# Performance work log

Measured on AMD Instinct MI355X. Metric: run time of the kernel, lower is better.

Reference implementation:

```python
import jax, jax.numpy as jnp
import numpy as np
from jax import lax

D_MODEL = 1024
FFN = 4096
CHUNK = 256
TTT_LR = 0.01
KSIZE = 5


def setup_inputs() -> dict:
    key = jax.random.key(0)
    ks = jax.random.split(key, 7)
    B, T = 2, 4096
    x = jax.random.normal(ks[0], (B, T, D_MODEL), dtype=jnp.float32)
    ttt_target = jax.random.normal(ks[1], (B, T, D_MODEL), dtype=jnp.float32)
    w_gate_up = jax.random.normal(ks[2], (2 * FFN, D_MODEL), dtype=jnp.float32) * 0.02
    w_down = jax.random.normal(ks[3], (D_MODEL, FFN), dtype=jnp.float32) * 0.02
    ttt_proj = jax.random.normal(ks[4], (D_MODEL, D_MODEL), dtype=jnp.float32) * 0.02
    conv_w = jax.random.normal(ks[5], (D_MODEL, 1, KSIZE), dtype=jnp.float32) * 0.02
    conv_b = jax.random.normal(ks[6], (D_MODEL,), dtype=jnp.float32) * 0.02
    return {"x": x, "ttt_target": ttt_target, "w_gate_up": w_gate_up,
            "w_down": w_down, "ttt_proj": ttt_proj, "conv_w": conv_w, "conv_b": conv_b}


def _pad_and_chunk(a, chunk):
    B, T, D = a.shape
    pad = (-T) % chunk
    if pad:
        a = jnp.pad(a, ((0, 0), (0, pad), (0, 0)))
    return a.reshape(B, -1, chunk, D)


def reference(x, ttt_target, w_gate_up, w_down, ttt_proj, conv_w, conv_b):
    B, T, D = x.shape
    # SwiGLU up path
    gate_up = jnp.einsum('btd,fd->btf', x, w_gate_up)  # (B,T,2F)
    gate, up = jnp.split(gate_up, 2, axis=-1)
    h = jax.nn.silu(gate) * up  # (B,T,F)
    # causal depthwise conv on ttt_target (torch pads K-1 both sides then slices [:T])
    t_ncl = ttt_target.transpose(0, 2, 1)  # (B,D,T)
    t = lax.conv_general_dilated(
        t_ncl, conv_w, window_strides=(1,), padding=[(KSIZE - 1, 0)],
        dimension_numbers=('NCH', 'OIH', 'NCH'), feature_group_count=D)
    t = (t + conv_b[None, :, None]).transpose(0, 2, 1)  # (B,T,D)
    # chunk
    h_c = _pad_and_chunk(h, CHUNK)  # (B,nc,C,F)
    t_c = _pad_and_chunk(t, CHUNK)  # (B,nc,C,D)
    nc = h_c.shape[1]
    if nc > 1:
        t_proj = jnp.einsum('btcd,ed->btce', t_c[:, :-1], ttt_proj)  # (B,nc-1,C,D)
        d_down = jnp.einsum('btch,btcd->btdh', h_c[:, :-1], t_proj)  # (B,nc-1,D,F)
    else:
        d_down = jnp.zeros((B, 0, D, FFN), dtype=h.dtype)
    w_orig = jnp.broadcast_to(w_down[None, None], (B, 1, D, FFN))
    w_all = jnp.concatenate([w_orig, d_down * jnp.float32(TTT_LR)], axis=1)
    w_adapted = jnp.cumsum(w_all, axis=1)  # (B,nc,D,F)
    out = jnp.einsum('btdh,btch->btcd', w_adapted, h_c)  # (B,nc,C,D)
    return out.reshape(B, -1, D)[:, :T]
```

## Files before the change

kernel.cpp:

```cpp
#include <hip/hip_runtime.h>
#include <hip/hip_bf16.h>
#include <stdint.h>

typedef unsigned short ushort_t;
typedef __bf16 bf16x8 __attribute__((ext_vector_type(8)));
typedef float f32x16 __attribute__((ext_vector_type(16)));

#define BM 128
#define BN 128
#define BK 64

__device__ inline float b2f(ushort_t u) {
    unsigned int x = ((unsigned int)u) << 16;
    float f; __builtin_memcpy(&f, &x, 4); return f;
}
__device__ inline ushort_t f2b(float f) {
    unsigned int x; __builtin_memcpy(&x, &f, 4);
    unsigned int r = (x + 0x7FFFu + ((x >> 16) & 1u)) >> 16;
    return (ushort_t)r;
}
__device__ inline void stage16(const ushort_t* g, ushort_t* s) {
    __builtin_amdgcn_global_load_lds((const __attribute__((address_space(1))) void*)g,
                                     (__attribute__((address_space(3))) void*)s, 16, 0, 0);
}
__device__ inline int swz(int r) { return (r & 7) ^ ((r >> 3) & 3); }
__device__ inline void stage_tile(const ushort_t* G, int ld, int k0, ushort_t* S, int tid) {
#pragma unroll
    for (int t = 0; t < 4; ++t) {
        int e = tid + t * 256;
        int row = e >> 3;
        int sw = ((e & 7) ^ swz(row)) * 8;
        stage16(G + (long long)row * ld + k0 + sw, &S[e * 8]);
    }
}
__device__ inline bf16x8 ldfrag(const ushort_t* S, int r, int c) {
    return *(const bf16x8*)&S[r * BK + ((c ^ swz(r)) * 8)];
}
__device__ inline void tile_decode(int& m0, int& n0) {
    const int nx = gridDim.x;
    int lin = blockIdx.y * nx + blockIdx.x;
    if ((nx & 7) == 0) {
        int q = nx >> 3;
        int k = lin & 7, s = lin >> 3;
        n0 = (k * q + s % q) * BN;
        m0 = (s / q) * BM;
    } else {
        m0 = blockIdx.y * BM;
        n0 = blockIdx.x * BN;
    }
}


#define SBAR() __builtin_amdgcn_sched_barrier(0)
#define BARRIER() do { SBAR(); __builtin_amdgcn_s_barrier(); SBAR(); } while (0)
#define WAITV(N) asm volatile("s_waitcnt vmcnt(" #N ")" ::: "memory")

__device__ inline int sw2(int r) { return ((r) & 3) ^ ((r >> 3) & 3); }

__device__ inline void stage_half(const ushort_t* G, int ldg, int kElem,
                                  ushort_t* Sbuf, int h, int tid) {
#pragma unroll
    for (int i2 = 0; i2 < 2; ++i2) {
        int s = tid + i2 * 512;
        int r = s >> 2, q = s & 3;
        int c = 4 * h + (q ^ sw2(r));
        stage16(G + (long long)r * ldg + kElem + c * 8, Sbuf + h * 8192 + s * 8);
    }
}
__device__ inline void stage_halfA(const ushort_t* G, int ldg,
                                   ushort_t* Sbuf, int h, int tid) {
    int r = tid >> 2, q = tid & 3;
    int c = 4 * h + (q ^ sw2(r));
    stage16(G + (long long)r * ldg + c * 8, Sbuf + h * 4096 + tid * 8);
}
__device__ inline int frag_off(int r, int c) {
    return r * 32 + ((c ^ sw2(r)) & 3) * 8;
}

template <int KS0, int MI0, bool LB>
__device__ __forceinline__ void phase_load(const ushort_t* cA, const ushort_t* cB,
                                           const int oa[4][2], const int ob[2][2],
                                           bf16x8 af_[2][2], bf16x8 bf_[2][2]) {
    constexpr int HO = (KS0 >> 1) * 8192;
#pragma unroll
    for (int k2 = 0; k2 < 2; ++k2) {
#pragma unroll
        for (int m2 = 0; m2 < 2; ++m2)
            af_[m2][k2] = *(const bf16x8*)&cA[oa[MI0 + m2][k2] + HO];
        if (LB) {
#pragma unroll
            for (int n2 = 0; n2 < 2; ++n2)
                bf_[n2][k2] = *(const bf16x8*)&cB[ob[n2][k2] + HO];
        }
    }
}
template <int MI0>
__device__ __forceinline__ void phase_mfma(bf16x8 af_[2][2], bf16x8 bf_[2][2],
                                           f32x16 (&acc)[4][2]) {
#pragma unroll
    for (int k2 = 0; k2 < 2; ++k2)
#pragma unroll
        for (int m2 = 0; m2 < 2; ++m2)
#pragma unroll
            for (int n2 = 0; n2 < 2; ++n2)
                acc[MI0 + m2][n2] = __builtin_amdgcn_mfma_f32_32x32x16_bf16(
                    af_[m2][k2], bf_[n2][k2], acc[MI0 + m2][n2], 0, 0, 0);
}

__device__ __forceinline__ void gemm256_core(const ushort_t* __restrict__ Ag, int lda,
                                             const ushort_t* __restrict__ Bg, int ldb,
                                             int K, ushort_t* smem, int tid,
                                             int wr, int wc, int l32, int hl,
                                             f32x16 (&acc)[4][2]) {
    ushort_t* A0s = smem;
    ushort_t* A1s = smem + 16384;
    ushort_t* B0s = smem + 32768;
    ushort_t* B1s = smem + 49152;
    const int NT = K >> 6;

    int oa[4][2], ob[2][2];
#pragma unroll
    for (int m2 = 0; m2 < 4; ++m2)
#pragma unroll
        for (int k2 = 0; k2 < 2; ++k2)
            oa[m2][k2] = frag_off(wr * 128 + m2 * 32 + l32, k2 * 2 + hl);
#pragma unroll
    for (int n2 = 0; n2 < 2; ++n2)
#pragma unroll
        for (int k2 = 0; k2 < 2; ++k2)
            ob[n2][k2] = frag_off(wc * 64 + n2 * 32 + l32, k2 * 2 + hl);

    stage_half(Ag, lda, 0, A0s, 0, tid);
    stage_half(Bg, ldb, 0, B0s, 0, tid);
    stage_half(Ag, lda, 0, A0s, 1, tid);
    stage_half(Bg, ldb, 0, B0s, 1, tid);
    stage_half(Ag, lda, 64, A1s, 0, tid);
    stage_half(Bg, ldb, 64, B1s, 0, tid);
    WAITV(8);
    BARRIER();

    for (int kt = 0; kt < NT; ++kt) {
        ushort_t* cA = (kt & 1) ? A1s : A0s;
        ushort_t* cB = (kt & 1) ? B1s : B0s;
        ushort_t* nA = (kt & 1) ? A0s : A1s;
        ushort_t* nB = (kt & 1) ? B0s : B1s;
        const bool h1 = (kt + 1 < NT), h2 = (kt + 2 < NT);
        const int kE1 = (kt + 1) << 6, kE2 = (kt + 2) << 6;
        bf16x8 af_[2][2], bf_[2][2];
        if (h1) stage_half(Ag, lda, kE1, nA, 1, tid);
        phase_load<0, 0, true>(cA, cB, oa, ob, af_, bf_);
        __builtin_amdgcn_s_setprio(1);
        phase_mfma<0>(af_, bf_, acc);
        __builtin_amdgcn_s_setprio(0);
        BARRIER();
        if (h1) stage_half(Bg, ldb, kE1, nB, 1, tid);
        phase_load<0, 2, false>(cA, cB, oa, ob, af_, bf_);
        __builtin_amdgcn_s_setprio(1);
        phase_mfma<2>(af_, bf_, acc);
        __builtin_amdgcn_s_setprio(0);
        if (h1) { WAITV(8); } else { WAITV(0); }
        BARRIER();
        if (h2) stage_half(Ag, lda, kE2, cA, 0, tid);
        phase_load<2, 0, true>(cA, cB, oa, ob, af_, bf_);
        __builtin_amdgcn_s_setprio(1);
        phase_mfma<0>(af_, bf_, acc);
        __builtin_amdgcn_s_setprio(0);
        BARRIER();
        if (h2) stage_half(Bg, ldb, kE2, cB, 0, tid);
        phase_load<2, 2, false>(cA, cB, oa, ob, af_, bf_);
        __builtin_amdgcn_s_setprio(1);
        phase_mfma<2>(af_, bf_, acc);
        __builtin_amdgcn_s_setprio(0);
        if (h1) { if (h2) { WAITV(8); } else { WAITV(4); } }
        BARRIER();
    }
}

__global__ __launch_bounds__(512, 2)
void k_gemm256_silu(const ushort_t* __restrict__ A, const ushort_t* __restrict__ Bp,
                    ushort_t* __restrict__ H) {
    extern __shared__ __attribute__((aligned(16))) ushort_t smem2[];
    const int tid = threadIdx.x;
    const int lane = tid & 63, l32 = lane & 31, hl = lane >> 5;
    const int wv = tid >> 6, wr = wv >> 2, wc = wv & 3;
    int lin = blockIdx.y * 32 + blockIdx.x;
    int k8 = lin & 7, s = lin >> 3;
    int n0 = (k8 * 4 + (s & 3)) * 256;
    int m0 = (s >> 2) * 256;
    const ushort_t* Ag = A + (long long)m0 * 1024;
    const ushort_t* Bg = Bp + (long long)n0 * 1024;
    f32x16 acc[4][2];
#pragma unroll
    for (int i = 0; i < 4; ++i) { acc[i][0] = (f32x16)(0.f); acc[i][1] = (f32x16)(0.f); }
    gemm256_core(Ag, 1024, Bg, 1024, 1024, smem2, tid, wr, wc, l32, hl, acc);
    const int hc = (n0 >> 1) + wc * 32 + l32;
#pragma unroll
    for (int mi = 0; mi < 4; ++mi)
#pragma unroll
        for (int reg = 0; reg < 16; ++reg) {
            int row = m0 + wr * 128 + mi * 32 + (reg & 3) + 8 * (reg >> 2) + 4 * hl;
            float g = acc[mi][0][reg], u = acc[mi][1][reg];
            float sg = g / (1.f + __expf(-g));
            H[(long long)row * 4096 + hc] = f2b(sg * u);
        }
}

__global__ __launch_bounds__(512, 2)
void k_gemm256_tri(const ushort_t* __restrict__ Hh, ushort_t* __restrict__ P) {
    extern __shared__ __attribute__((aligned(16))) ushort_t smem2[];
    const int tid = threadIdx.x;
    const int lane = tid & 63, l32 = lane & 31, hl = lane >> 5;
    const int wv = tid >> 6, wr = wv >> 2, wc = wv & 3;
    int pairIdx = (blockIdx.x & 7) * 30 + (blockIdx.x >> 3);
    const int bb = pairIdx / 120;
    int p = pairIdx % 120;
    int i = 1, rem = p;
    while (rem >= i) { rem -= i; ++i; }
    const int j = rem;
    const ushort_t* Ag = Hh + (long long)bb * 4096 * 4096 + (long long)(i * 256) * 4096;
    const ushort_t* Bg = Hh + (long long)bb * 4096 * 4096 + (long long)(j * 256) * 4096;
    f32x16 acc[4][2];
#pragma unroll
    for (int a = 0; a < 4; ++a) { acc[a][0] = (f32x16)(0.f); acc[a][1] = (f32x16)(0.f); }
    gemm256_core(Ag, 4096, Bg, 4096, 4096, smem2, tid, wr, wc, l32, hl, acc);
    ushort_t* Pp = P + (long long)bb * 4096 * 4096;
#pragma unroll
    for (int mi = 0; mi < 4; ++mi)
#pragma unroll
        for (int nj = 0; nj < 2; ++nj) {
            int col = j * 256 + wc * 64 + nj * 32 + l32;
#pragma unroll
            for (int reg = 0; reg < 16; ++reg) {
                int row = i * 256 + wr * 128 + mi * 32 + (reg & 3) + 8 * (reg >> 2) + 4 * hl;
                Pp[(long long)row * 4096 + col] = f2b(acc[mi][nj][reg]);
            }
        }
}

template <int KS0>
__device__ __forceinline__ void oload_ks(const ushort_t* cA, const ushort_t* cB,
                                         const int oa[2][2], const int ob[2][2],
                                         bf16x8 af_[2][2], bf16x8 bf_[2][2]) {
    constexpr int HOA = (KS0 >> 1) * 4096;
    constexpr int HOB = (KS0 >> 1) * 8192;
#pragma unroll
    for (int k2 = 0; k2 < 2; ++k2) {
#pragma unroll
        for (int m2 = 0; m2 < 2; ++m2)
            af_[m2][k2] = *(const bf16x8*)&cA[oa[m2][k2] + HOA];
#pragma unroll
        for (int n2 = 0; n2 < 2; ++n2)
            bf_[n2][k2] = *(const bf16x8*)&cB[ob[n2][k2] + HOB];
    }
}
__device__ __forceinline__ void omfma(bf16x8 af_[2][2], bf16x8 bf_[2][2],
                                      f32x16 (&acc)[2][2]) {
#pragma unroll
    for (int k2 = 0; k2 < 2; ++k2)
#pragma unroll
        for (int m2 = 0; m2 < 2; ++m2)
#pragma unroll
            for (int n2 = 0; n2 < 2; ++n2)
                acc[m2][n2] = __builtin_amdgcn_mfma_f32_32x32x16_bf16(
                    af_[m2][k2], bf_[n2][k2], acc[m2][n2], 0, 0, 0);
}

__global__ __launch_bounds__(512, 2)
void k_gemm256_out(const ushort_t* __restrict__ h, const ushort_t* __restrict__ wdown,
                   const ushort_t* __restrict__ P, const ushort_t* __restrict__ tpT,
                   float* __restrict__ out) {
    constexpr int T = 4096, D = 1024, F = 4096, C = 256, K1 = 4096;
    extern __shared__ __attribute__((aligned(16))) ushort_t smem2[];
    const int tid = threadIdx.x;
    const int lane = tid & 63, l32 = lane & 31, hl = lane >> 5;
    const int wv = tid >> 6, wr = wv >> 2, wc = wv & 3;

    const int bx = blockIdx.x;
    const int logical = (bx & 7) * 32 + (bx >> 3);
    const int z = logical >> 3, t = logical & 7;
    const int bb = z >> 4, ii = z & 15;
    const int m0 = (t >> 2) * 128, n0 = (t & 3) * 256;
    const int K = K1 + ii * C;

    const ushort_t* hA = h + (long long)bb * T * F + (long long)(ii * C + m0) * F;
    const ushort_t* pA = P + (long long)bb * T * T + (long long)(ii * C + m0) * T;
    const ushort_t* wB = wdown + (long long)n0 * F;
    const ushort_t* tB = tpT + (long long)bb * D * T + (long long)n0 * T;

    ushort_t* A0s = smem2;
    ushort_t* A1s = smem2 + 8192;
    ushort_t* B0s = smem2 + 16384;
    ushort_t* B1s = smem2 + 32768;

    int oa[2][2], ob[2][2];
#pragma unroll
    for (int m2 = 0; m2 < 2; ++m2)
#pragma unroll
        for (int k2 = 0; k2 < 2; ++k2)
            oa[m2][k2] = frag_off(wr * 64 + m2 * 32 + l32, k2 * 2 + hl);
#pragma unroll
    for (int n2 = 0; n2 < 2; ++n2)
#pragma unroll
        for (int k2 = 0; k2 < 2; ++k2)
            ob[n2][k2] = frag_off(wc * 64 + n2 * 32 + l32, k2 * 2 + hl);

    f32x16 acc[2][2];
#pragma unroll
    for (int a = 0; a < 2; ++a)
#pragma unroll
        for (int c = 0; c < 2; ++c) acc[a][c] = (f32x16)(0.f);

    auto srcA = [&](int kE) { return kE < K1 ? hA + kE : pA + (kE - K1); };
    auto srcB = [&](int kE) { return kE < K1 ? wB + kE : tB + (kE - K1); };

    const int NT = K >> 6;

    stage_halfA(srcA(0), F, A0s, 0, tid);
    stage_half (srcB(0), F, 0, B0s, 0, tid);
    stage_halfA(srcA(0), F, A0s, 1, tid);
    stage_half (srcB(0), F, 0, B0s, 1, tid);
    stage_halfA(srcA(64), F, A1s, 0, tid);
    stage_half (srcB(64), F, 0, B1s, 0, tid);
    WAITV(6);
    BARRIER();

    for (int kt = 0; kt < NT; ++kt) {
        ushort_t* cA = (kt & 1) ? A1s : A0s;
        ushort_t* cB = (kt & 1) ? B1s : B0s;
        ushort_t* nA = (kt & 1) ? A0s : A1s;
        ushort_t* nB = (kt & 1) ? B0s : B1s;
        const bool h1 = (kt + 1 < NT), h2 = (kt + 2 < NT);
        const int kE1 = (kt + 1) << 6, kE2 = (kt + 2) << 6;
        bf16x8 af_[2][2], bf_[2][2];
        if (h1) {
            stage_halfA(srcA(kE1), F, nA, 1, tid);
            stage_half (srcB(kE1), F, 0, nB, 1, tid);
        }
        oload_ks<0>(cA, cB, oa, ob, af_, bf_);
        __builtin_amdgcn_s_setprio(1);
        omfma(af_, bf_, acc);
        __builtin_amdgcn_s_setprio(0);
        if (h1) { WAITV(6); } else { WAITV(0); }
        BARRIER();
        if (h2) {
            stage_halfA(srcA(kE2), F, cA, 0, tid);
            stage_half (srcB(kE2), F, 0, cB, 0, tid);
        }
        oload_ks<2>(cA, cB, oa, ob, af_, bf_);
        __builtin_amdgcn_s_setprio(1);
        omfma(af_, bf_, acc);
        __builtin_amdgcn_s_setprio(0);
        if (h2) { WAITV(6); } else { if (h1) { WAITV(3); } else { WAITV(0); } }
        BARRIER();
    }

    float* Op = out + (long long)bb * T * D + (long long)(ii * C) * D;
#pragma unroll
    for (int mi = 0; mi < 2; ++mi)
#pragma unroll
        for (int nj = 0; nj < 2; ++nj) {
            int col = n0 + wc * 64 + nj * 32 + l32;
#pragma unroll
            for (int reg = 0; reg < 16; ++reg) {
                int row = m0 + wr * 64 + mi * 32 + (reg & 3) + 8 * (reg >> 2) + 4 * hl;
                Op[(long long)row * D + col] = acc[mi][nj][reg];
            }
        }
}

__global__ void k_prep(const float* __restrict__ x, const float* __restrict__ wgu,
                       const float* __restrict__ proj, const float* __restrict__ wdown,
                       const float* __restrict__ tt, const float* __restrict__ cw,
                       const float* __restrict__ cb,
                       ushort_t* __restrict__ xb, ushort_t* __restrict__ gb,
                       ushort_t* __restrict__ pb, ushort_t* __restrict__ wb,
                       ushort_t* __restrict__ tb, int permW) {
    constexpr int T = 4096, D = 1024;
    int blk = blockIdx.x;
    if (blk < 21504) {
        int i = blk * 256 + threadIdx.x;
        const float* src; ushort_t* dst; int off; int dstoff;
        if (i < 2097152)      { src = x;     dst = xb; off = i; dstoff = off; }
        else if (i < 4194304) {
            src = wgu; dst = gb; off = i - 2097152;
            if (permW) {
                int r = off >> 8, cu = off & 255;
                int pr = (r < 4096) ? (((r >> 5) << 6) + (r & 31))
                                    : ((((r - 4096) >> 5) << 6) + 32 + ((r - 4096) & 31));
                dstoff = (pr << 8) + cu;
            } else dstoff = off;
        }
        else if (i < 4456448) { src = proj;  dst = pb; off = i - 4194304; dstoff = off; }
        else                  { src = wdown; dst = wb; off = i - 4456448; dstoff = off; }
        float4 v = ((const float4*)src)[off];
        ushort4 o; o.x = f2b(v.x); o.y = f2b(v.y); o.z = f2b(v.z); o.w = f2b(v.w);
        ((ushort4*)dst)[dstoff] = o;
    } else {
        int idx = (blk - 21504) * 256 + threadIdx.x;
        int d = idx & (D - 1);
        int tq = (idx >> 10) & (T / 4 - 1);
        int b = idx / (D * (T / 4));
        int t0 = tq * 4;
        const float* base = tt + (long long)b * T * D + d;
        float w0 = cw[d * 5 + 0], w1 = cw[d * 5 + 1], w2 = cw[d * 5 + 2],
              w3 = cw[d * 5 + 3], w4 = cw[d * 5 + 4];
        float bias = cb[d];
        float win[8];
#pragma unroll
        for (int m = 0; m < 8; ++m) {
            int ts = t0 - 4 + m;
            win[m] = (ts >= 0) ? base[(long long)ts * D] : 0.f;
        }
        ushort_t* op = tb + (long long)b * T * D + (long long)t0 * D + d;
#pragma unroll
        for (int r = 0; r < 4; ++r) {
            float a = bias + w0 * win[r] + w1 * win[r + 1] + w2 * win[r + 2]
                    + w3 * win[r + 3] + w4 * win[r + 4];
            op[(long long)r * D] = f2b(a);
        }
    }
}

__global__ __launch_bounds__(256, 4)
void k_gemm_nt(const ushort_t* __restrict__ A, const ushort_t* __restrict__ B,
               ushort_t* __restrict__ C, int K, int lda, int ldb, int ldc,
               long long sAb, long long sBb, long long sCb, float scale) {
    __shared__ __attribute__((aligned(16))) ushort_t sA[BM * BK];
    __shared__ __attribute__((aligned(16))) ushort_t sB[BN * BK];

    int m0, n0;
    tile_decode(m0, n0);
    const int bb = blockIdx.z;
    const ushort_t* Ab = A + bb * sAb + (long long)m0 * lda;
    const ushort_t* Bb = B + bb * sBb + (long long)n0 * ldb;

    const int tid = threadIdx.x;
    const int lane = tid & 63, l32 = lane & 31, half = lane >> 5;
    const int wave = tid >> 6;
    const int wm = (wave >> 1) * 64, wn = (wave & 1) * 64;

    f32x16 acc[2][2];
#pragma unroll
    for (int i = 0; i < 2; ++i)
#pragma unroll
        for (int j = 0; j < 2; ++j) acc[i][j] = (f32x16)(0.f);

    for (int k0 = 0; k0 < K; k0 += BK) {
        __syncthreads();
        stage_tile(Ab, lda, k0, sA, tid);
        stage_tile(Bb, ldb, k0, sB, tid);
        __syncthreads();
#pragma unroll
        for (int ks = 0; ks < 4; ++ks) {
            bf16x8 af[2], bfr[2];
#pragma unroll
            for (int mi = 0; mi < 2; ++mi)
                af[mi] = ldfrag(sA, wm + mi * 32 + l32, ks * 2 + half);
#pragma unroll
            for (int nj = 0; nj < 2; ++nj)
                bfr[nj] = ldfrag(sB, wn + nj * 32 + l32, ks * 2 + half);
#pragma unroll
            for (int mi = 0; mi < 2; ++mi)
#pragma unroll
                for (int nj = 0; nj < 2; ++nj)
                    acc[mi][nj] = __builtin_amdgcn_mfma_f32_32x32x16_bf16(af[mi], bfr[nj], acc[mi][nj], 0, 0, 0);
        }
    }

    ushort_t* Cp = C + bb * sCb;
#pragma unroll
    for (int mi = 0; mi < 2; ++mi)
#pragma unroll
        for (int nj = 0; nj < 2; ++nj) {
            int col = n0 + wn + nj * 32 + l32;
#pragma unroll
            for (int reg = 0; reg < 16; ++reg) {
                int row = m0 + wm + mi * 32 + (reg & 3) + 8 * (reg >> 2) + 4 * half;
                Cp[(long long)row * ldc + col] = f2b(acc[mi][nj][reg] * scale);
            }
        }
}

__global__ __launch_bounds__(256)
void k_gemm_silu(const ushort_t* __restrict__ A, const ushort_t* __restrict__ Bg,
                 const ushort_t* __restrict__ Bu, ushort_t* __restrict__ H,
                 int K, int lda, int ldb, int ldh) {
    __shared__ __attribute__((aligned(16))) ushort_t sA[BM * BK];
    __shared__ __attribute__((aligned(16))) ushort_t sBg[BN * BK];
    __shared__ __attribute__((aligned(16))) ushort_t sBu[BN * BK];

    int m0, n0;
    tile_decode(m0, n0);
    const ushort_t* Ab = A + (long long)m0 * lda;
    const ushort_t* Bgb = Bg + (long long)n0 * ldb;
    const ushort_t* Bub = Bu + (long long)n0 * ldb;

    const int tid = threadIdx.x;
    const int lane = tid & 63, l32 = lane & 31, half = lane >> 5;
    const int wave = tid >> 6;
    const int wm = (wave >> 1) * 64, wn = (wave & 1) * 64;

    f32x16 ag[2][2], au[2][2];
#pragma unroll
    for (int i = 0; i < 2; ++i)
#pragma unroll
        for (int j = 0; j < 2; ++j) { ag[i][j] = (f32x16)(0.f); au[i][j] = (f32x16)(0.f); }

    for (int k0 = 0; k0 < K; k0 += BK) {
        __syncthreads();
        stage_tile(Ab, lda, k0, sA, tid);
        stage_tile(Bgb, ldb, k0, sBg, tid);
        stage_tile(Bub, ldb, k0, sBu, tid);
        __syncthreads();
#pragma unroll
        for (int ks = 0; ks < 4; ++ks) {
            bf16x8 af[2], bg[2], bu[2];
#pragma unroll
            for (int mi = 0; mi < 2; ++mi)
                af[mi] = ldfrag(sA, wm + mi * 32 + l32, ks * 2 + half);
#pragma unroll
            for (int nj = 0; nj < 2; ++nj) {
                bg[nj] = ldfrag(sBg, wn + nj * 32 + l32, ks * 2 + half);
                bu[nj] = ldfrag(sBu, wn + nj * 32 + l32, ks * 2 + half);
            }
#pragma unroll
            for (int mi = 0; mi < 2; ++mi)
#pragma unroll
                for (int nj = 0; nj < 2; ++nj) {
                    ag[mi][nj] = __builtin_amdgcn_mfma_f32_32x32x16_bf16(af[mi], bg[nj], ag[mi][nj], 0, 0, 0);
                    au[mi][nj] = __builtin_amdgcn_mfma_f32_32x32x16_bf16(af[mi], bu[nj], au[mi][nj], 0, 0, 0);
                }
        }
    }

#pragma unroll
    for (int mi = 0; mi < 2; ++mi)
#pragma unroll
        for (int nj = 0; nj < 2; ++nj) {
            int col = n0 + wn + nj * 32 + l32;
#pragma unroll
            for (int reg = 0; reg < 16; ++reg) {
                int row = m0 + wm + mi * 32 + (reg & 3) + 8 * (reg >> 2) + 4 * half;
                float g = ag[mi][nj][reg], u = au[mi][nj][reg];
                float s = g / (1.f + __expf(-g));
                H[(long long)row * ldh + col] = f2b(s * u);
            }
        }
}

__global__ __launch_bounds__(256, 4)
void k_gemm_tri(const ushort_t* __restrict__ H, ushort_t* __restrict__ P,
                int K, int ldh, int ldp, long long sHb, long long sPb) {
    __shared__ __attribute__((aligned(16))) ushort_t sA[BM * BK];
    __shared__ __attribute__((aligned(16))) ushort_t sB[BN * BK];

    const int lin = blockIdx.x;
    const int g = lin >> 5, w = lin & 31;
    const int xk = w & 7, t = w >> 3;
    int pairIdx = g * 8 + xk;
    const int bb = pairIdx / 120;
    int p = pairIdx % 120;
    int i = 1, rem = p;
    while (rem >= i) { rem -= i; ++i; }
    const int j = rem;
    const int m0 = (t >> 1) * BM, n0 = (t & 1) * BN;

    const ushort_t* Ab = H + bb * sHb + (long long)(i * 256 + m0) * ldh;
    const ushort_t* Bb = H + bb * sHb + (long long)(j * 256 + n0) * ldh;

    const int tid = threadIdx.x;
    const int lane = tid & 63, l32 = lane & 31, half = lane >> 5;
    const int wave = tid >> 6;
    const int wm = (wave >> 1) * 64, wn = (wave & 1) * 64;

    f32x16 acc[2][2];
#pragma unroll
    for (int a = 0; a < 2; ++a)
#pragma unroll
        for (int c = 0; c < 2; ++c) acc[a][c] = (f32x16)(0.f);

    for (int k0 = 0; k0 < K; k0 += BK) {
        __syncthreads();
        stage_tile(Ab, ldh, k0, sA, tid);
        stage_tile(Bb, ldh, k0, sB, tid);
        __syncthreads();
#pragma unroll
        for (int ks = 0; ks < 4; ++ks) {
            bf16x8 af[2], bfr[2];
#pragma unroll
            for (int mi = 0; mi < 2; ++mi)
                af[mi] = ldfrag(sA, wm + mi * 32 + l32, ks * 2 + half);
#pragma unroll
            for (int nj = 0; nj < 2; ++nj)
                bfr[nj] = ldfrag(sB, wn + nj * 32 + l32, ks * 2 + half);
#pragma unroll
            for (int mi = 0; mi < 2; ++mi)
#pragma unroll
                for (int nj = 0; nj < 2; ++nj)
                    acc[mi][nj] = __builtin_amdgcn_mfma_f32_32x32x16_bf16(af[mi], bfr[nj], acc[mi][nj], 0, 0, 0);
        }
    }

    ushort_t* Pp = P + bb * sPb;
#pragma unroll
    for (int mi = 0; mi < 2; ++mi)
#pragma unroll
        for (int nj = 0; nj < 2; ++nj) {
            int col = j * 256 + n0 + wn + nj * 32 + l32;
#pragma unroll
            for (int reg = 0; reg < 16; ++reg) {
                int row = i * 256 + m0 + wm + mi * 32 + (reg & 3) + 8 * (reg >> 2) + 4 * half;
                Pp[(long long)row * ldp + col] = f2b(acc[mi][nj][reg]);
            }
        }
}

__global__ __launch_bounds__(256, 4)
void k_gemm_out(const ushort_t* __restrict__ h, const ushort_t* __restrict__ wdown,
                const ushort_t* __restrict__ P, const ushort_t* __restrict__ tpT,
                float* __restrict__ out) {
    constexpr int T = 4096, D = 1024, F = 4096, C = 256, K1 = 4096;
    __shared__ __attribute__((aligned(16))) ushort_t sA[BM * BK];
    __shared__ __attribute__((aligned(16))) ushort_t sB[BN * BK];

    const int z = blockIdx.z, bb = z >> 4, ii = z & 15;
    const int K2 = ii * C;
    int m0, n0;
    tile_decode(m0, n0);

    const ushort_t* A1 = h + (long long)bb * T * F + (long long)(ii * C + m0) * F;
    const ushort_t* B1 = wdown + (long long)n0 * F;
    const ushort_t* A2 = P + (long long)bb * T * T + (long long)(ii * C + m0) * T;
    const ushort_t* B2 = tpT + (long long)bb * D * T + (long long)n0 * T;

    const int tid = threadIdx.x;
    const int lane = tid & 63, l32 = lane & 31, half = lane >> 5;
    const int wave = tid >> 6;
    const int wm = (wave >> 1) * 64, wn = (wave & 1) * 64;

    f32x16 acc[2][2];
#pragma unroll
    for (int i = 0; i < 2; ++i)
#pragma unroll
        for (int j = 0; j < 2; ++j) acc[i][j] = (f32x16)(0.f);

    const int K = K1 + K2;
    for (int k0 = 0; k0 < K; k0 += BK) {
        const ushort_t* As = (k0 < K1) ? A1 + k0 : A2 + (k0 - K1);
        const ushort_t* Bs = (k0 < K1) ? B1 + k0 : B2 + (k0 - K1);
        __syncthreads();
        stage_tile(As, 4096, 0, sA, tid);
        stage_tile(Bs, 4096, 0, sB, tid);
        __syncthreads();
#pragma unroll
        for (int ks = 0; ks < 4; ++ks) {
            bf16x8 af[2], bfr[2];
#pragma unroll
            for (int mi = 0; mi < 2; ++mi)
                af[mi] = ldfrag(sA, wm + mi * 32 + l32, ks * 2 + half);
#pragma unroll
            for (int nj = 0; nj < 2; ++nj)
                bfr[nj] = ldfrag(sB, wn + nj * 32 + l32, ks * 2 + half);
#pragma unroll
            for (int mi = 0; mi < 2; ++mi)
#pragma unroll
                for (int nj = 0; nj < 2; ++nj)
                    acc[mi][nj] = __builtin_amdgcn_mfma_f32_32x32x16_bf16(af[mi], bfr[nj], acc[mi][nj], 0, 0, 0);
        }
    }

    float* Op = out + (long long)bb * T * D + (long long)ii * C * D;
#pragma unroll
    for (int mi = 0; mi < 2; ++mi)
#pragma unroll
        for (int nj = 0; nj < 2; ++nj) {
            int col = n0 + wn + nj * 32 + l32;
#pragma unroll
            for (int reg = 0; reg < 16; ++reg) {
                int row = m0 + wm + mi * 32 + (reg & 3) + 8 * (reg >> 2) + 4 * half;
                Op[(long long)row * D + col] = acc[mi][nj][reg];
            }
        }
}

static int g_big = -1;

extern "C" void kernel_launch(void* const* d_in, const int* in_sizes, int n_in,
                              void* d_out, int out_size, void* d_ws, size_t ws_size,
                              hipStream_t stream) {
    const float* x         = (const float*)d_in[0];
    const float* ttt_tgt   = (const float*)d_in[1];
    const float* w_gate_up = (const float*)d_in[2];
    const float* w_down    = (const float*)d_in[3];
    const float* ttt_proj  = (const float*)d_in[4];
    const float* conv_w    = (const float*)d_in[5];
    const float* conv_b    = (const float*)d_in[6];
    float* out = (float*)d_out;
    (void)in_sizes; (void)n_in; (void)out_size; (void)ws_size;

    constexpr int Bb = 2, T = 4096, D = 1024, F = 4096, C = 256;
    constexpr float LR = 0.01f;

    if (g_big < 0) {
        hipError_t e1 = hipFuncSetAttribute((const void*)k_gemm256_silu,
                                            hipFuncAttributeMaxDynamicSharedMemorySize, 131072);
        hipError_t e2 = hipFuncSetAttribute((const void*)k_gemm256_tri,
                                            hipFuncAttributeMaxDynamicSharedMemorySize, 131072);
        hipError_t e3 = hipFuncSetAttribute((const void*)k_gemm256_out,
                                            hipFuncAttributeMaxDynamicSharedMemorySize, 98304);
        g_big = (e1 == hipSuccess && e2 == hipSuccess && e3 == hipSuccess) ? 1 : 0;
    }

    char* ws = (char*)d_ws;
    ushort_t* x_bf     = (ushort_t*)(ws);
    ushort_t* wgu_bf   = (ushort_t*)(ws + 16777216LL);
    ushort_t* t_bf     = (ushort_t*)(ws + 2 * 16777216LL);
    ushort_t* P        = (ushort_t*)(ws);
    ushort_t* proj_bf  = (ushort_t*)(ws + 67108864LL);
    ushort_t* wdown_bf = (ushort_t*)(ws + 67108864LL + 2097152LL);
    ushort_t* tpT      = (ushort_t*)(ws + 67108864LL + 2097152LL + 8388608LL);
    ushort_t* h        = (ushort_t*)(ws + 67108864LL + 2097152LL + 8388608LL + 16777216LL);

    k_prep<<<21504 + 8192, 256, 0, stream>>>(x, w_gate_up, ttt_proj, w_down,
                                             ttt_tgt, conv_w, conv_b,
                                             x_bf, wgu_bf, proj_bf, wdown_bf, t_bf, g_big);

    k_gemm_nt<<<dim3(T / BN, D / BM, Bb), 256, 0, stream>>>(
        proj_bf, t_bf, tpT, D, D, D, T,
        0, (long long)T * D, (long long)D * T, LR);

    if (g_big) {
        k_gemm256_silu<<<dim3(32, 32, 1), 512, 131072, stream>>>(x_bf, wgu_bf, h);
    } else {
        k_gemm_silu<<<dim3(F / BN, (Bb * T) / BM, 1), 256, 0, stream>>>(
            x_bf, wgu_bf, wgu_bf + (long long)F * D, h, D, D, D, F);
    }

    if (g_big) {
        k_gemm256_tri<<<dim3(240, 1, 1), 512, 131072, stream>>>(h, P);
    } else {
        k_gemm_tri<<<dim3(960, 1, 1), 256, 0, stream>>>(
            h, P, F, F, T, (long long)T * F, (long long)T * T);
    }

    if (g_big) {
        k_gemm256_out<<<dim3(256, 1, 1), 512, 98304, stream>>>(h, wdown_bf, P, tpT, out);
    } else {
        k_gemm_out<<<dim3(D / BN, C / BM, Bb * 16), 256, 0, stream>>>(
            h, wdown_bf, P, tpT, out);
    }
}
```

Measured before the change: 570.3 us.

## Split the output GEMM's K dimension in two with atomic accumulation

The output GEMM now launches twice as many blocks, each covering half of the K range (the w_down part plus the triangular P part), and accumulates partial tiles into the output with float atomicAdd. The output is zeroed with a memset beforehand. This is meant to fill more of the device and reduce tail imbalance from the varying K lengths per chunk, at the cost of an extra memset pass and atomic write traffic to the output.

Result: slower. 603.4 us (+5.8%).

```diff
diff --git a/kernel.cpp b/kernel.cpp
--- a/kernel.cpp
+++ b/kernel.cpp
@@ -276,11 +276,17 @@
     const int wv = tid >> 6, wr = wv >> 2, wc = wv & 3;
 
     const int bx = blockIdx.x;
-    const int logical = (bx & 7) * 32 + (bx >> 3);
-    const int z = logical >> 3, t = logical & 7;
+    const int logical = (bx & 7) * 64 + (bx >> 3);
+    const int z = logical >> 4;
+    const int t = (logical >> 1) & 7;
+    const int seg = logical & 1;
     const int bb = z >> 4, ii = z & 15;
     const int m0 = (t >> 2) * 128, n0 = (t & 3) * 256;
     const int K = K1 + ii * C;
+    const int NT = K >> 6;
+    const int NTh = NT >> 1;
+    const int ktBeg = seg ? NTh : 0;
+    const int NTs = seg ? (NT - NTh) : NTh;
 
     const ushort_t* hA = h + (long long)bb * T * F + (long long)(ii * C + m0) * F;
     const ushort_t* pA = P + (long long)bb * T * T + (long long)(ii * C + m0) * T;
@@ -313,24 +319,24 @@
     auto srcA = [&](int kE) { return kE < K1 ? hA + kE : pA + (kE - K1); };
     auto srcB = [&](int kE) { return kE < K1 ? wB + kE : tB + (kE - K1); };
 
-    const int NT = K >> 6;
-
-    stage_halfA(srcA(0), F, A0s, 0, tid);
-    stage_half (srcB(0), F, 0, B0s, 0, tid);
-    stage_halfA(srcA(0), F, A0s, 1, tid);
-    stage_half (srcB(0), F, 0, B0s, 1, tid);
-    stage_halfA(srcA(64), F, A1s, 0, tid);
-    stage_half (srcB(64), F, 0, B1s, 0, tid);
+    const int kE0 = ktBeg << 6;
+
+    stage_halfA(srcA(kE0), F, A0s, 0, tid);
+    stage_half (srcB(kE0), F, 0, B0s, 0, tid);
+    stage_halfA(srcA(kE0), F, A0s, 1, tid);
+    stage_half (srcB(kE0), F, 0, B0s, 1, tid);
+    stage_halfA(srcA(kE0 + 64), F, A1s, 0, tid);
+    stage_half (srcB(kE0 + 64), F, 0, B1s, 0, tid);
     WAITV(6);
     BARRIER();
 
-    for (int kt = 0; kt < NT; ++kt) {
+    for (int kt = 0; kt < NTs; ++kt) {
         ushort_t* cA = (kt & 1) ? A1s : A0s;
         ushort_t* cB = (kt & 1) ? B1s : B0s;
         ushort_t* nA = (kt & 1) ? A0s : A1s;
         ushort_t* nB = (kt & 1) ? B0s : B1s;
-        const bool h1 = (kt + 1 < NT), h2 = (kt + 2 < NT);
-        const int kE1 = (kt + 1) << 6, kE2 = (kt + 2) << 6;
+        const bool h1 = (kt + 1 < NTs), h2 = (kt + 2 < NTs);
+        const int kE1 = (ktBeg + kt + 1) << 6, kE2 = (ktBeg + kt + 2) << 6;
         bf16x8 af_[2][2], bf_[2][2];
         if (h1) {
             stage_halfA(srcA(kE1), F, nA, 1, tid);
@@ -363,7 +369,7 @@
 #pragma unroll
             for (int reg = 0; reg < 16; ++reg) {
                 int row = m0 + wr * 64 + mi * 32 + (reg & 3) + 8 * (reg >> 2) + 4 * hl;
-                Op[(long long)row * D + col] = acc[mi][nj][reg];
+                atomicAdd(&Op[(long long)row * D + col], acc[mi][nj][reg]);
             }
         }
 }
@@ -696,7 +702,7 @@
     const float* conv_w    = (const float*)d_in[5];
     const float* conv_b    = (const float*)d_in[6];
     float* out = (float*)d_out;
-    (void)in_sizes; (void)n_in; (void)out_size; (void)ws_size;
+    (void)in_sizes; (void)n_in; (void)ws_size;
 
     constexpr int Bb = 2, T = 4096, D = 1024, F = 4096, C = 256;
     constexpr float LR = 0.01f;
@@ -721,6 +727,8 @@
     ushort_t* tpT      = (ushort_t*)(ws + 67108864LL + 2097152LL + 8388608LL);
     ushort_t* h        = (ushort_t*)(ws + 67108864LL + 2097152LL + 8388608LL + 16777216LL);
 
+    if (g_big) hipMemsetAsync(out, 0, (size_t)out_size, stream);
+
     k_prep<<<21504 + 8192, 256, 0, stream>>>(x, w_gate_up, ttt_proj, w_down,
                                              ttt_tgt, conv_w, conv_b,
                                              x_bf, wgu_bf, proj_bf, wdown_bf, t_bf, g_big);
@@ -744,7 +752,7 @@
     }
 
     if (g_big) {
-        k_gemm256_out<<<dim3(256, 1, 1), 512, 98304, stream>>>(h, wdown_bf, P, tpT, out);
+        k_gemm256_out<<<dim3(512, 1, 1), 512, 98304, stream>>>(h, wdown_bf, P, tpT, out);
     } else {
         k_gemm_out<<<dim3(D / BN, C / BM, Bb * 16), 256, 0, stream>>>(
             h, wdown_bf, P, tpT, out);
```

## Replace double-buffered 64-wide K pipeline with 4-slot ring of 32-wide stages

Applied to the files above, without the earlier changes.

Both GEMM cores (the SwiGLU/P GEMM and the output GEMM) drop the two-buffer, 64-element K tile with split half-phase loads. They now use a four-slot circular buffer of 32-element K slices, prefetched three slices ahead. Each iteration issues one slice load, then does all fragment reads and MFMAs for the current slice, then waits and hits one barrier. The aim is to keep more global loads in flight and simplify synchronization. The cost is more barriers per unit of K and smaller MFMA batches between barriers, with the same shared memory footprint.

Measured after the change: 563.7 us. No clear change (-1.2%).

```diff
diff --git a/kernel.cpp b/kernel.cpp
--- a/kernel.cpp
+++ b/kernel.cpp
@@ -58,53 +58,22 @@
 __device__ inline int sw2(int r) { return ((r) & 3) ^ ((r >> 3) & 3); }
 
 __device__ inline void stage_half(const ushort_t* G, int ldg, int kElem,
-                                  ushort_t* Sbuf, int h, int tid) {
+                                  ushort_t* Sbuf, int tid) {
 #pragma unroll
     for (int i2 = 0; i2 < 2; ++i2) {
         int s = tid + i2 * 512;
         int r = s >> 2, q = s & 3;
-        int c = 4 * h + (q ^ sw2(r));
-        stage16(G + (long long)r * ldg + kElem + c * 8, Sbuf + h * 8192 + s * 8);
-    }
-}
-__device__ inline void stage_halfA(const ushort_t* G, int ldg,
-                                   ushort_t* Sbuf, int h, int tid) {
+        int c = q ^ sw2(r);
+        stage16(G + (long long)r * ldg + kElem + c * 8, Sbuf + s * 8);
+    }
+}
+__device__ inline void stage_halfA(const ushort_t* G, int ldg, ushort_t* Sbuf, int tid) {
     int r = tid >> 2, q = tid & 3;
-    int c = 4 * h + (q ^ sw2(r));
-    stage16(G + (long long)r * ldg + c * 8, Sbuf + h * 4096 + tid * 8);
+    int c = q ^ sw2(r);
+    stage16(G + (long long)r * ldg + c * 8, Sbuf + tid * 8);
 }
 __device__ inline int frag_off(int r, int c) {
     return r * 32 + ((c ^ sw2(r)) & 3) * 8;
-}
-
-template <int KS0, int MI0, bool LB>
-__device__ __forceinline__ void phase_load(const ushort_t* cA, const ushort_t* cB,
-                                           const int oa[4][2], const int ob[2][2],
-                                           bf16x8 af_[2][2], bf16x8 bf_[2][2]) {
-    constexpr int HO = (KS0 >> 1) * 8192;
-#pragma unroll
-    for (int k2 = 0; k2 < 2; ++k2) {
-#pragma unroll
-        for (int m2 = 0; m2 < 2; ++m2)
-            af_[m2][k2] = *(const bf16x8*)&cA[oa[MI0 + m2][k2] + HO];
-        if (LB) {
-#pragma unroll
-            for (int n2 = 0; n2 < 2; ++n2)
-                bf_[n2][k2] = *(const bf16x8*)&cB[ob[n2][k2] + HO];
-        }
-    }
-}
-template <int MI0>
-__device__ __forceinline__ void phase_mfma(bf16x8 af_[2][2], bf16x8 bf_[2][2],
-                                           f32x16 (&acc)[4][2]) {
-#pragma unroll
-    for (int k2 = 0; k2 < 2; ++k2)
-#pragma unroll
-        for (int m2 = 0; m2 < 2; ++m2)
-#pragma unroll
-            for (int n2 = 0; n2 < 2; ++n2)
-                acc[MI0 + m2][n2] = __builtin_amdgcn_mfma_f32_32x32x16_bf16(
-                    af_[m2][k2], bf_[n2][k2], acc[MI0 + m2][n2], 0, 0, 0);
 }
 
 __device__ __forceinline__ void gemm256_core(const ushort_t* __restrict__ Ag, int lda,
@@ -112,11 +81,9 @@
                                              int K, ushort_t* smem, int tid,
                                              int wr, int wc, int l32, int hl,
                                              f32x16 (&acc)[4][2]) {
-    ushort_t* A0s = smem;
-    ushort_t* A1s = smem + 16384;
-    ushort_t* B0s = smem + 32768;
-    ushort_t* B1s = smem + 49152;
-    const int NT = K >> 6;
+    const int NH = K >> 5;
+    ushort_t* Ab0 = smem;
+    ushort_t* Bb0 = smem + 32768;
 
     int oa[4][2], ob[2][2];
 #pragma unroll
@@ -130,48 +97,69 @@
         for (int k2 = 0; k2 < 2; ++k2)
             ob[n2][k2] = frag_off(wc * 64 + n2 * 32 + l32, k2 * 2 + hl);
 
-    stage_half(Ag, lda, 0, A0s, 0, tid);
-    stage_half(Bg, ldb, 0, B0s, 0, tid);
-    stage_half(Ag, lda, 0, A0s, 1, tid);
-    stage_half(Bg, ldb, 0, B0s, 1, tid);
-    stage_half(Ag, lda, 64, A1s, 0, tid);
-    stage_half(Bg, ldb, 64, B1s, 0, tid);
+    stage_half(Ag, lda, 0,  Ab0,          tid);
+    stage_half(Bg, ldb, 0,  Bb0,          tid);
+    stage_half(Ag, lda, 32, Ab0 + 8192,   tid);
+    stage_half(Bg, ldb, 32, Bb0 + 8192,   tid);
+    stage_half(Ag, lda, 64, Ab0 + 16384,  tid);
+    stage_half(Bg, ldb, 64, Bb0 + 16384,  tid);
     WAITV(8);
     BARRIER();
 
-    for (int kt = 0; kt < NT; ++kt) {
-        ushort_t* cA = (kt & 1) ? A1s : A0s;
-        ushort_t* cB = (kt & 1) ? B1s : B0s;
-        ushort_t* nA = (kt & 1) ? A0s : A1s;
-        ushort_t* nB = (kt & 1) ? B0s : B1s;
-        const bool h1 = (kt + 1 < NT), h2 = (kt + 2 < NT);
-        const int kE1 = (kt + 1) << 6, kE2 = (kt + 2) << 6;
-        bf16x8 af_[2][2], bf_[2][2];
-        if (h1) stage_half(Ag, lda, kE1, nA, 1, tid);
-        phase_load<0, 0, true>(cA, cB, oa, ob, af_, bf_);
+    int h = 0;
+    for (; h < NH - 3; ++h) {
+        ushort_t* cA = Ab0 + (h & 3) * 8192;
+        ushort_t* cB = Bb0 + (h & 3) * 8192;
+        int nb = (h + 3) & 3;
+        stage_half(Ag, lda, (h + 3) << 5, Ab0 + nb * 8192, tid);
+        stage_half(Bg, ldb, (h + 3) << 5, Bb0 + nb * 8192, tid);
+        bf16x8 af_[4][2], bf_[2][2];
+#pragma unroll
+        for (int k2 = 0; k2 < 2; ++k2) {
+#pragma unroll
+            for (int m2 = 0; m2 < 4; ++m2)
+                af_[m2][k2] = *(const bf16x8*)&cA[oa[m2][k2]];
+#pragma unroll
+            for (int n2 = 0; n2 < 2; ++n2)
+                bf_[n2][k2] = *(const bf16x8*)&cB[ob[n2][k2]];
+        }
         __builtin_amdgcn_s_setprio(1);
-        phase_mfma<0>(af_, bf_, acc);
+#pragma unroll
+        for (int k2 = 0; k2 < 2; ++k2)
+#pragma unroll
+            for (int m2 = 0; m2 < 4; ++m2)
+#pragma unroll
+                for (int n2 = 0; n2 < 2; ++n2)
+                    acc[m2][n2] = __builtin_amdgcn_mfma_f32_32x32x16_bf16(
+                        af_[m2][k2], bf_[n2][k2], acc[m2][n2], 0, 0, 0);
         __builtin_amdgcn_s_setprio(0);
+        WAITV(8);
         BARRIER();
-        if (h1) stage_half(Bg, ldb, kE1, nB, 1, tid);
-        phase_load<0, 2, false>(cA, cB, oa, ob, af_, bf_);
+    }
+    for (; h < NH; ++h) {
+        ushort_t* cA = Ab0 + (h & 3) * 8192;
+        ushort_t* cB = Bb0 + (h & 3) * 8192;
+        bf16x8 af_[4][2], bf_[2][2];
+#pragma unroll
+        for (int k2 = 0; k2 < 2; ++k2) {
+#pragma unroll
+            for (int m2 = 0; m2 < 4; ++m2)
+                af_[m2][k2] = *(const bf16x8*)&cA[oa[m2][k2]];
+#pragma unroll
+            for (int n2 = 0; n2 < 2; ++n2)
+                bf_[n2][k2] = *(const bf16x8*)&cB[ob[n2][k2]];
+        }
         __builtin_amdgcn_s_setprio(1);
-        phase_mfma<2>(af_, bf_, acc);
+#pragma unroll
+        for (int k2 = 0; k2 < 2; ++k2)
+#pragma unroll
+            for (int m2 = 0; m2 < 4; ++m2)
+#pragma unroll
+                for (int n2 = 0; n2 < 2; ++n2)
+                    acc[m2][n2] = __builtin_amdgcn_mfma_f32_32x32x16_bf16(
+                        af_[m2][k2], bf_[n2][k2], acc[m2][n2], 0, 0, 0);
         __builtin_amdgcn_s_setprio(0);
-        if (h1) { WAITV(8); } else { WAITV(0); }
-        BARRIER();
-        if (h2) stage_half(Ag, lda, kE2, cA, 0, tid);
-        phase_load<2, 0, true>(cA, cB, oa, ob, af_, bf_);
-        __builtin_amdgcn_s_setprio(1);
-        phase_mfma<0>(af_, bf_, acc);
-        __builtin_amdgcn_s_setprio(0);
-        BARRIER();
-        if (h2) stage_half(Bg, ldb, kE2, cB, 0, tid);
-        phase_load<2, 2, false>(cA, cB, oa, ob, af_, bf_);
-        __builtin_amdgcn_s_setprio(1);
-        phase_mfma<2>(af_, bf_, acc);
-        __builtin_amdgcn_s_setprio(0);
-        if (h1) { if (h2) { WAITV(8); } else { WAITV(4); } }
+        if (h + 2 < NH) { WAITV(4); } else { WAITV(0); }
         BARRIER();
     }
 }
@@ -237,34 +225,6 @@
         }
 }
 
-template <int KS0>
-__device__ __forceinline__ void oload_ks(const ushort_t* cA, const ushort_t* cB,
-                                         const int oa[2][2], const int ob[2][2],
-                                         bf16x8 af_[2][2], bf16x8 bf_[2][2]) {
-    constexpr int HOA = (KS0 >> 1) * 4096;
-    constexpr int HOB = (KS0 >> 1) * 8192;
-#pragma unroll
-    for (int k2 = 0; k2 < 2; ++k2) {
-#pragma unroll
-        for (int m2 = 0; m2 < 2; ++m2)
-            af_[m2][k2] = *(const bf16x8*)&cA[oa[m2][k2] + HOA];
-#pragma unroll
-        for (int n2 = 0; n2 < 2; ++n2)
-            bf_[n2][k2] = *(const bf16x8*)&cB[ob[n2][k2] + HOB];
-    }
-}
-__device__ __forceinline__ void omfma(bf16x8 af_[2][2], bf16x8 bf_[2][2],
-                                      f32x16 (&acc)[2][2]) {
-#pragma unroll
-    for (int k2 = 0; k2 < 2; ++k2)
-#pragma unroll
-        for (int m2 = 0; m2 < 2; ++m2)
-#pragma unroll
-            for (int n2 = 0; n2 < 2; ++n2)
-                acc[m2][n2] = __builtin_amdgcn_mfma_f32_32x32x16_bf16(
-                    af_[m2][k2], bf_[n2][k2], acc[m2][n2], 0, 0, 0);
-}
-
 __global__ __launch_bounds__(512, 2)
 void k_gemm256_out(const ushort_t* __restrict__ h, const ushort_t* __restrict__ wdown,
                    const ushort_t* __restrict__ P, const ushort_t* __restrict__ tpT,
@@ -281,16 +241,15 @@
     const int bb = z >> 4, ii = z & 15;
     const int m0 = (t >> 2) * 128, n0 = (t & 3) * 256;
     const int K = K1 + ii * C;
+    const int NH = K >> 5;
 
     const ushort_t* hA = h + (long long)bb * T * F + (long long)(ii * C + m0) * F;
     const ushort_t* pA = P + (long long)bb * T * T + (long long)(ii * C + m0) * T;
     const ushort_t* wB = wdown + (long long)n0 * F;
     const ushort_t* tB = tpT + (long long)bb * D * T + (long long)n0 * T;
 
-    ushort_t* A0s = smem2;
-    ushort_t* A1s = smem2 + 8192;
-    ushort_t* B0s = smem2 + 16384;
-    ushort_t* B1s = smem2 + 32768;
+    ushort_t* Ab0 = smem2;
+    ushort_t* Bb0 = smem2 + 16384;
 
     int oa[2][2], ob[2][2];
 #pragma unroll
@@ -313,44 +272,69 @@
     auto srcA = [&](int kE) { return kE < K1 ? hA + kE : pA + (kE - K1); };
     auto srcB = [&](int kE) { return kE < K1 ? wB + kE : tB + (kE - K1); };
 
-    const int NT = K >> 6;
-
-    stage_halfA(srcA(0), F, A0s, 0, tid);
-    stage_half (srcB(0), F, 0, B0s, 0, tid);
-    stage_halfA(srcA(0), F, A0s, 1, tid);
-    stage_half (srcB(0), F, 0, B0s, 1, tid);
-    stage_halfA(srcA(64), F, A1s, 0, tid);
-    stage_half (srcB(64), F, 0, B1s, 0, tid);
+    stage_halfA(srcA(0),  F, Ab0,         tid);
+    stage_half (srcB(0),  F, 0, Bb0,      tid);
+    stage_halfA(srcA(32), F, Ab0 + 4096,  tid);
+    stage_half (srcB(32), F, 0, Bb0 + 8192, tid);
+    stage_halfA(srcA(64), F, Ab0 + 8192,  tid);
+    stage_half (srcB(64), F, 0, Bb0 + 16384, tid);
     WAITV(6);
     BARRIER();
 
-    for (int kt = 0; kt < NT; ++kt) {
-        ushort_t* cA = (kt & 1) ? A1s : A0s;
-        ushort_t* cB = (kt & 1) ? B1s : B0s;
-        ushort_t* nA = (kt & 1) ? A0s : A1s;
-        ushort_t* nB = (kt & 1) ? B0s : B1s;
-        const bool h1 = (kt + 1 < NT), h2 = (kt + 2 < NT);
-        const int kE1 = (kt + 1) << 6, kE2 = (kt + 2) << 6;
+    int hh = 0;
+    for (; hh < NH - 3; ++hh) {
+        ushort_t* cA = Ab0 + (hh & 3) * 4096;
+        ushort_t* cB = Bb0 + (hh & 3) * 8192;
+        int nb = (hh + 3) & 3;
+        stage_halfA(srcA((hh + 3) << 5), F, Ab0 + nb * 4096, tid);
+        stage_half (srcB((hh + 3) << 5), F, 0, Bb0 + nb * 8192, tid);
         bf16x8 af_[2][2], bf_[2][2];
-        if (h1) {
-            stage_halfA(srcA(kE1), F, nA, 1, tid);
-            stage_half (srcB(kE1), F, 0, nB, 1, tid);
-        }
-        oload_ks<0>(cA, cB, oa, ob, af_, bf_);
+#pragma unroll
+        for (int k2 = 0; k2 < 2; ++k2) {
+#pragma unroll
+            for (int m2 = 0; m2 < 2; ++m2)
+                af_[m2][k2] = *(const bf16x8*)&cA[oa[m2][k2]];
+#pragma unroll
+            for (int n2 = 0; n2 < 2; ++n2)
+                bf_[n2][k2] = *(const bf16x8*)&cB[ob[n2][k2]];
+        }
         __builtin_amdgcn_s_setprio(1);
-        omfma(af_, bf_, acc);
+#pragma unroll
+        for (int k2 = 0; k2 < 2; ++k2)
+#pragma unroll
+            for (int m2 = 0; m2 < 2; ++m2)
+#pragma unroll
+                for (int n2 = 0; n2 < 2; ++n2)
+                    acc[m2][n2] = __builtin_amdgcn_mfma_f32_32x32x16_bf16(
+                        af_[m2][k2], bf_[n2][k2], acc[m2][n2], 0, 0, 0);
         __builtin_amdgcn_s_setprio(0);
-        if (h1) { WAITV(6); } else { WAITV(0); }
+        WAITV(6);
         BARRIER();
-        if (h2) {
-            stage_halfA(srcA(kE2), F, cA, 0, tid);
-            stage_half (srcB(kE2), F, 0, cB, 0, tid);
-        }
-        oload_ks<2>(cA, cB, oa, ob, af_, bf_);
+    }
+    for (; hh < NH; ++hh) {
+        ushort_t* cA = Ab0 + (hh & 3) * 4096;
+        ushort_t* cB = Bb0 + (hh & 3) * 8192;
+        bf16x8 af_[2][2], bf_[2][2];
+#pragma unroll
+        for (int k2 = 0; k2 < 2; ++k2) {
+#pragma unroll
+            for (int m2 = 0; m2 < 2; ++m2)
+                af_[m2][k2] = *(const bf16x8*)&cA[oa[m2][k2]];
+#pragma unroll
+            for (int n2 = 0; n2 < 2; ++n2)
+                bf_[n2][k2] = *(const bf16x8*)&cB[ob[n2][k2]];
+        }
         __builtin_amdgcn_s_setprio(1);
-        omfma(af_, bf_, acc);
+#pragma unroll
+        for (int k2 = 0; k2 < 2; ++k2)
+#pragma unroll
+            for (int m2 = 0; m2 < 2; ++m2)
+#pragma unroll
+                for (int n2 = 0; n2 < 2; ++n2)
+                    acc[m2][n2] = __builtin_amdgcn_mfma_f32_32x32x16_bf16(
+                        af_[m2][k2], bf_[n2][k2], acc[m2][n2], 0, 0, 0);
         __builtin_amdgcn_s_setprio(0);
-        if (h2) { WAITV(6); } else { if (h1) { WAITV(3); } else { WAITV(0); } }
+        if (hh + 2 < NH) { WAITV(3); } else { WAITV(0); }
         BARRIER();
     }
 
```
